# Performance work log

Measured on AMD Instinct MI355X. Metric: run time of the kernel, lower is better.

The kernel has to match this reference:

```python
import jax, jax.numpy as jnp
import numpy as np

OMEGA_ENC = 0.01   # Encoder.omega
OMEGA_K = 0.1      # KernelMLP.omega
N0, E0 = 4096, 16384     # level-0 graph
N1, E1 = 1024, 8192      # level-1 (pooled) graph
F_IN, H, LAT, DIM = 8, 64, 32, 3
F = H + DIM              # conv input features (x || pos)


def _glorot(key, shape):
    s = jnp.sqrt(2.0 / (shape[0] + shape[-1]))
    return (jax.random.normal(key, shape) * s).astype(jnp.float32)


def setup_inputs() -> dict:
    key = jax.random.key(0)
    ks = jax.random.split(key, 24)
    inp = {
        "x": jax.random.normal(ks[0], (N0, F_IN), jnp.float32),
        "pos": jax.random.normal(ks[1], (N0, DIM), jnp.float32),
        "edge_index": jax.random.randint(ks[2], (2, E0), 0, N0),
        "pool_edge_index1": jax.random.randint(ks[3], (2, E1), 0, N1),
        "pool_pos1": jax.random.normal(ks[4], (N1, DIM), jnp.float32),
        "pool_keep_idx0": jnp.sort(jax.random.randint(ks[5], (N1,), 0, N0)),
        "lin0_w": _glorot(ks[6], (F_IN, H)),
        "lin0_b": 0.01 * jax.random.normal(ks[7], (H,), jnp.float32),
        "lin1_w": _glorot(ks[8], (H, LAT)),
        "lin1_b": 0.01 * jax.random.normal(ks[9], (LAT,), jnp.float32),
    }
    k = 10
    for i in range(2):
        inp[f"conv{i}_k_w0"] = _glorot(ks[k], (DIM + 1, H))
        inp[f"conv{i}_k_b0"] = 0.01 * jax.random.normal(ks[k + 1], (H,), jnp.float32)
        inp[f"conv{i}_k_w1"] = _glorot(ks[k + 2], (H, H))
        inp[f"conv{i}_k_b1"] = 0.01 * jax.random.normal(ks[k + 3], (H,), jnp.float32)
        inp[f"conv{i}_k_w2"] = _glorot(ks[k + 4], (H, F))
        inp[f"conv{i}_k_b2"] = 0.01 * jax.random.normal(ks[k + 5], (F,), jnp.float32)
        inp[f"conv{i}_bias"] = jnp.zeros((H,), jnp.float32)  # zeros() init in torch
        k += 6
    return inp


def _with_self_loops(ei, n):
    # add_remaining_self_loops: input edges are assumed self-loop-free
    loops = jnp.arange(n, dtype=ei.dtype)
    return jnp.concatenate([ei, jnp.stack([loops, loops])], axis=1)


def _kernel_conv(xf, ei, pos, n, w0, b0, w1, b1, w2, b2, bias):
    src, dst = ei[0], ei[1]
    rel = pos[dst] - pos[src]                               # [E,3]
    zero = jnp.all(rel == 0.0, axis=1)                      # self loops -> rho=0, nan phi in torch
    rel_s = jnp.where(zero[:, None], 1.0, rel)              # safe values (avoid nan grads)
    rho = jnp.sqrt(jnp.sum(rel_s * rel_s, axis=1))
    theta = jnp.arctan2(rel_s[:, 1], rel_s[:, 0])
    phi = jnp.arcsin(jnp.clip(rel_s[:, 2] / rho, -1.0, 1.0))
    # torch sets theta/phi to 0 where phi is nan (rho==0); rho itself is 0 there
    rho = jnp.where(zero, 0.0, rho)
    theta = jnp.where(zero, 0.0, theta)
    phi = jnp.where(zero, 0.0, phi)
    feats = jnp.stack([rho, theta / jnp.pi, phi / jnp.pi], axis=1)   # [E,3]
    # KernelMLP lin0 on (feats || channel_id), evaluated for all out channels at once
    base = feats @ w0[:DIM] + b0                            # [E,H]
    ch = jnp.arange(H, dtype=xf.dtype)                      # out_channels == H
    h0 = jnp.sin(OMEGA_K * (base[None] + ch[:, None, None] * w0[DIM][None, None]))  # [C,E,H]
    h1 = jnp.sin(OMEGA_K * (jnp.einsum('ceh,hk->cek', h0, w1) + b1))                # [C,E,H]
    x_j = xf[src]                                           # [E,F]
    # msg[e,c] = (lin2(h1[c,e]) * x_j[e]).sum(); lin2 folded into the contraction
    msg = jnp.einsum('ceh,hf,ef->ec', h1, w2, x_j) + (x_j @ b2)[:, None]            # [E,C]
    return jax.ops.segment_sum(msg, dst, num_segments=n) + bias


def reference(x, edge_index, pos, pool_edge_index1, pool_pos1, pool_keep_idx0,
              lin0_w, lin0_b, lin1_w, lin1_b,
              conv0_k_w0, conv0_k_b0, conv0_k_w1, conv0_k_b1, conv0_k_w2, conv0_k_b2, conv0_bias,
              conv1_k_w0, conv1_k_b0, conv1_k_w1, conv1_k_b1, conv1_k_w2, conv1_k_b2, conv1_bias):
    n0 = x.shape[0]
    h = jnp.sin(OMEGA_ENC * (x @ lin0_w + lin0_b))
    ei0 = _with_self_loops(edge_index, n0)
    h = jnp.sin(OMEGA_ENC * _kernel_conv(jnp.concatenate([h, pos], 1), ei0, pos, n0,
                                         conv0_k_w0, conv0_k_b0, conv0_k_w1, conv0_k_b1,
                                         conv0_k_w2, conv0_k_b2, conv0_bias))
    # max_pool_neighbor_x: per-node max over neighbors incl. self (self loops in ei0)
    h = jax.ops.segment_max(h[ei0[0]], ei0[1], num_segments=n0)[pool_keep_idx0]
    n1 = pool_pos1.shape[0]
    ei1 = _with_self_loops(pool_edge_index1, n1)
    h = jnp.sin(OMEGA_ENC * _kernel_conv(jnp.concatenate([h, pool_pos1], 1), ei1, pool_pos1, n1,
                                         conv1_k_w0, conv1_k_b0, conv1_k_w1, conv1_k_b1,
                                         conv1_k_w2, conv1_k_b2, conv1_bias))
    return jnp.sin(OMEGA_ENC * (h @ lin1_w + lin1_b))   # [N1, LAT]
```

## Files before the change

kernel.cpp:

```cpp
#include <hip/hip_runtime.h>
#include <hip/hip_fp16.h>

#define N0C 4096
#define E0C 16384
#define N1C 1024
#define E1C 8192
#define HC 64
#define FINC 8
#define LATC 32
#define FC 67
#define E0T (E0C + N0C)
#define E1T (E1C + N1C)

typedef float f32x4 __attribute__((ext_vector_type(4)));
typedef _Float16 f16x8 __attribute__((ext_vector_type(8)));

__global__ __launch_bounds__(256) void k_prep(
    const float* __restrict__ x, const float* __restrict__ l0w,
    const float* __restrict__ l0b, const float* __restrict__ posp,
    const float* __restrict__ c0w2, const float* __restrict__ c0b2,
    const float* __restrict__ c0w0, const float* __restrict__ c1w0,
    const float* __restrict__ c0w1, const float* __restrict__ c1w1,
    _Float16* __restrict__ bC0, _Float16* __restrict__ bS0,
    _Float16* __restrict__ bC1, _Float16* __restrict__ bS1,
    _Float16* __restrict__ w1f0, _Float16* __restrict__ w1f1,
    float* __restrict__ tN, float* __restrict__ dN,
    float* __restrict__ accz) {
  if (blockIdx.x < 256) {
    __shared__ float w2s[64][69];
    __shared__ float xr[4][64];
    const int tid = threadIdx.x;
    const int wave = __builtin_amdgcn_readfirstlane(tid >> 6), lane = tid & 63;
    for (int idx = tid; idx < HC * FC; idx += 256)
      w2s[idx / FC][idx % FC] = c0w2[idx];
    __syncthreads();
#pragma unroll
    for (int i = 0; i < 4; ++i) {
      const int n = (blockIdx.x * 4 + wave) + i * 1024;
      float a = l0b[lane];
#pragma unroll
      for (int f = 0; f < FINC; ++f) a = fmaf(x[n * FINC + f], l0w[f * HC + lane], a);
      xr[wave][lane] = sinf(0.01f * a);
      __builtin_amdgcn_wave_barrier();
      const float px = posp[n * 3], py = posp[n * 3 + 1], pz = posp[n * 3 + 2];
      float tl = 0.f, ds = 0.f;
#pragma unroll 8
      for (int f = 0; f < HC; ++f) {
        float xv = xr[wave][f];
        tl = fmaf(xv, w2s[lane][f], tl);
        ds = fmaf(xv, c0b2[f], ds);
      }
      tl = fmaf(px, w2s[lane][64], fmaf(py, w2s[lane][65], fmaf(pz, w2s[lane][66], tl)));
      ds = fmaf(px, c0b2[64], fmaf(py, c0b2[65], fmaf(pz, c0b2[66], ds)));
      tN[n * HC + lane] = tl;
      if (lane == 0) dN[n] = ds;
      __builtin_amdgcn_wave_barrier();
    }
  } else if (blockIdx.x < 320) {
    int id = (blockIdx.x - 256) * 256 + threadIdx.x;
    if (id < 8192) {
      int lvl = id >> 12, r = id & 4095;
      int fi = r >> 9, lane = (r >> 3) & 63, j = r & 7;
      int nt = fi & 3, ks = fi >> 2;
      int c = nt * 16 + (lane & 15);
      int h = ks * 32 + (lane >> 4) * 8 + j;
      const float* w = lvl ? c1w0 : c0w0;
      float s, cv;
      sincosf(0.1f * (float)c * w[3 * HC + h], &s, &cv);
      (lvl ? bC1 : bC0)[r] = (_Float16)cv;
      (lvl ? bS1 : bS0)[r] = (_Float16)s;
    } else {
      int r0 = id - 8192;
      int lvl = r0 >> 12, r = r0 & 4095;
      int fi = r >> 9, lane = (r >> 3) & 63, j = r & 7;
      int ms = fi & 3, ks = fi >> 2;
      int h = ks * 32 + (lane >> 4) * 8 + j;
      int kout = ms * 16 + (lane & 15);
      const float* w = lvl ? c1w1 : c0w1;
      (lvl ? w1f1 : w1f0)[r] = (_Float16)(0.1f * w[h * HC + kout]);
    }
  } else {
    int t = (blockIdx.x - 320) * 256 + threadIdx.x;
    f32x4 z = {0.f, 0.f, 0.f, 0.f};
    f32x4* zp = (f32x4*)accz;
    zp[t] = z;
    zp[t + 49152] = z;
    zp[t + 98304] = z;
  }
}

template <bool L1>
__global__ __launch_bounds__(256, 3) void k_conv(
    const int* __restrict__ ei, int E, int eTot,
    const float* __restrict__ posp,
    const float* __restrict__ tN, const float* __restrict__ dN,
    const unsigned* __restrict__ pooled, const int* __restrict__ keep,
    const float* __restrict__ w2, const float* __restrict__ b2,
    const float* __restrict__ kw0, const float* __restrict__ kb0,
    const _Float16* __restrict__ bC, const _Float16* __restrict__ bS,
    const _Float16* __restrict__ w1f, const float* __restrict__ b1,
    float* __restrict__ acc_out) {
  __shared__ __attribute__((aligned(16))) _Float16 bCs[4096], bSs[4096];
  __shared__ __attribute__((aligned(16))) _Float16 scS[4][2][64], scC[4][2][64];
  __shared__ float w2s[64][69];
  __shared__ float xrs[4][2][64];
  __shared__ float trow[4][64];
  const int tid = threadIdx.x;
  const int wave = __builtin_amdgcn_readfirstlane(tid >> 6), lane = tid & 63;
  const int q = lane >> 4;
  for (int idx = tid; idx < 512; idx += 256) {
    ((f16x8*)bCs)[idx] = ((const f16x8*)bC)[idx];
    ((f16x8*)bSs)[idx] = ((const f16x8*)bS)[idx];
  }
  if constexpr (L1) {
    for (int idx = tid; idx < HC * FC; idx += 256)
      w2s[idx / FC][idx % FC] = w2[idx];
  }
  f16x8 w1r[8];
#pragma unroll
  for (int f = 0; f < 8; ++f) w1r[f] = *(const f16x8*)(w1f + ((f << 6) + lane) * 8);
  f32x4 bbq[4];
#pragma unroll
  for (int ms = 0; ms < 4; ++ms) {
    f32x4 t = *(const f32x4*)(b1 + ms * 16 + q * 4);
    bbq[ms] = t * 0.1f;
  }
  const float kb0v = kb0[lane];
  const float kw0x = kw0[lane], kw0y = kw0[HC + lane], kw0z = kw0[2 * HC + lane];
  float b2v = 0.f, b2x = 0.f, b2y = 0.f, b2z = 0.f;
  if constexpr (L1) {
    b2v = b2[lane];
    b2x = b2[64]; b2y = b2[65]; b2z = b2[66];
  }
  __syncthreads();

  const int nW = gridDim.x * 4;
  int e = blockIdx.x * 4 + wave;
  if (e >= eTot) return;

  auto stg = [&](int ee, int bufIdx, int& sN, int& dTo, float& sv, float& cv,
                 float& dv, float& opx, float& opy, float& opz) {
    int s, d2;
    if (ee < E) { s = ei[ee]; d2 = ei[E + ee]; } else { s = ee - E; d2 = s; }
    sN = s;
    dTo = d2;
    const float px = posp[s * 3], py = posp[s * 3 + 1], pz = posp[s * 3 + 2];
    const float rx = posp[d2 * 3] - px;
    const float ry = posp[d2 * 3 + 1] - py;
    const float rz = posp[d2 * 3 + 2] - pz;
    opx = px; opy = py; opz = pz;
    float f0 = 0.f, f1 = 0.f, f2 = 0.f;
    if (!(rx == 0.f && ry == 0.f && rz == 0.f)) {
      const float INV_PI = 0.3183098861837907f;
      const float PI_F = 3.14159265358979f;
      const float PI_2 = 1.5707963267948966f;
      float rho = sqrtf(rx * rx + ry * ry + rz * rz);
      float ax = fabsf(rx), ay = fabsf(ry);
      float mx = fmaxf(ax, ay), mn = fminf(ax, ay);
      float zr = mn * __builtin_amdgcn_rcpf(mx);
      float z2 = zr * zr;
      float pa = fmaf(z2, -0.0040540580f, 0.0218612288f);
      pa = fmaf(z2, pa, -0.0559098861f);
      pa = fmaf(z2, pa, 0.0964200441f);
      pa = fmaf(z2, pa, -0.1390853351f);
      pa = fmaf(z2, pa, 0.1994653599f);
      pa = fmaf(z2, pa, -0.3332985605f);
      pa = fmaf(z2, pa, 0.9999993329f);
      float at = pa * zr;
      at = (ay > ax) ? (PI_2 - at) : at;
      at = (rx < 0.f) ? (PI_F - at) : at;
      float th = copysignf(at, ry);
      float zz = rz * __builtin_amdgcn_rcpf(rho);
      float az = fminf(fabsf(zz), 1.0f);
      float sq = sqrtf(1.0f - az);
      float pp = fmaf(az, -0.0187293f, 0.0742610f);
      pp = fmaf(az, pp, -0.2121144f);
      pp = fmaf(az, pp, 1.5707288f);
      float as = PI_2 - sq * pp;
      float ph = copysignf(as, zz);
      f0 = rho; f1 = th * INV_PI; f2 = ph * INV_PI;
    }
    float base = fmaf(f0, kw0x, fmaf(f1, kw0y, fmaf(f2, kw0z, kb0v)));
    __sincosf(0.1f * base, &sv, &cv);
    if constexpr (L1) {
      int kn = keep[s];
      unsigned key = pooled[(size_t)kn * HC + lane];
      unsigned bb = (key & 0x80000000u) ? (key & 0x7FFFFFFFu) : ~key;
      float xv = __uint_as_float(bb);
      xrs[wave][bufIdx][lane] = xv;
      float dp = xv * b2v;
      dp += __shfl_xor(dp, 1, 64);  dp += __shfl_xor(dp, 2, 64);
      dp += __shfl_xor(dp, 4, 64);  dp += __shfl_xor(dp, 8, 64);
      dp += __shfl_xor(dp, 16, 64); dp += __shfl_xor(dp, 32, 64);
      dv = dp + fmaf(px, b2x, fmaf(py, b2y, pz * b2z));
    } else {
      dv = dN[s];
    }
  };

  int s0, d0;
  float sv0, cv0, dv0, p0x, p0y, p0z;
  stg(e, 0, s0, d0, sv0, cv0, dv0, p0x, p0y, p0z);
  int buf = 0;
  scS[wave][0][lane] = (_Float16)sv0;
  scC[wave][0][lane] = (_Float16)cv0;
  __builtin_amdgcn_wave_barrier();

  while (true) {
    const int en = e + nW;
    const bool more = en < eTot;
    int s1 = 0, d1 = 0;
    float sv1 = 0.f, cv1 = 0.f, dv1 = 0.f, p1x = 0.f, p1y = 0.f, p1z = 0.f;
    if (more) {
      stg(en, buf ^ 1, s1, d1, sv1, cv1, dv1, p1x, p1y, p1z);
      scS[wave][buf ^ 1][lane] = (_Float16)sv1;
      scC[wave][buf ^ 1][lane] = (_Float16)cv1;
    }
    __builtin_amdgcn_wave_barrier();

    f32x4 tr[4];
    if constexpr (L1) {
      float tl = 0.f;
#pragma unroll 8
      for (int f = 0; f < HC; ++f) tl = fmaf(xrs[wave][buf][f], w2s[lane][f], tl);
      tl = fmaf(p0x, w2s[lane][64],
           fmaf(p0y, w2s[lane][65], fmaf(p0z, w2s[lane][66], tl)));
      trow[wave][lane] = tl;
      __builtin_amdgcn_wave_barrier();
#pragma unroll
      for (int ms = 0; ms < 4; ++ms)
        tr[ms] = *(const f32x4*)&trow[wave][ms * 16 + q * 4];
      __builtin_amdgcn_wave_barrier();
    } else {
      const float* trp = tN + (size_t)s0 * HC;
#pragma unroll
      for (int ms = 0; ms < 4; ++ms) tr[ms] = *(const f32x4*)(trp + ms * 16 + q * 4);
    }

    f32x4 acc[4][4];
#pragma unroll
    for (int ms = 0; ms < 4; ++ms)
#pragma unroll
      for (int nt = 0; nt < 4; ++nt) acc[ms][nt] = bbq[ms];
#pragma unroll
    for (int ks = 0; ks < 2; ++ks) {
      f16x8 sv8 = *(const f16x8*)&scS[wave][buf][ks * 32 + q * 8];
      f16x8 cv8 = *(const f16x8*)&scC[wave][buf][ks * 32 + q * 8];
      f16x8 bf[4];
#pragma unroll
      for (int nt = 0; nt < 4; ++nt) {
        f16x8 cb = *(const f16x8*)&bCs[((ks * 4 + nt) * 64 + lane) * 8];
        f16x8 sb = *(const f16x8*)&bSs[((ks * 4 + nt) * 64 + lane) * 8];
        bf[nt] = sv8 * cb + cv8 * sb;
      }
#pragma unroll
      for (int ms = 0; ms < 4; ++ms)
#pragma unroll
        for (int nt = 0; nt < 4; ++nt)
          acc[ms][nt] = __builtin_amdgcn_mfma_f32_16x16x32_f16(
              w1r[ks * 4 + ms], bf[nt], acc[ms][nt], 0, 0, 0);
    }

    float snt0 = 0.f, snt1 = 0.f, snt2 = 0.f, snt3 = 0.f;
#pragma unroll
    for (int ms = 0; ms < 4; ++ms) {
#pragma unroll
      for (int r = 0; r < 4; ++r) {
        float tt = tr[ms][r];
        snt0 = fmaf(__sinf(acc[ms][0][r]), tt, snt0);
        snt1 = fmaf(__sinf(acc[ms][1][r]), tt, snt1);
        snt2 = fmaf(__sinf(acc[ms][2][r]), tt, snt2);
        snt3 = fmaf(__sinf(acc[ms][3][r]), tt, snt3);
      }
    }
    snt0 += __shfl_xor(snt0, 16, 64); snt0 += __shfl_xor(snt0, 32, 64);
    snt1 += __shfl_xor(snt1, 16, 64); snt1 += __shfl_xor(snt1, 32, 64);
    snt2 += __shfl_xor(snt2, 16, 64); snt2 += __shfl_xor(snt2, 32, 64);
    snt3 += __shfl_xor(snt3, 16, 64); snt3 += __shfl_xor(snt3, 32, 64);
    float val = (q == 0) ? snt0 : (q == 1) ? snt1 : (q == 2) ? snt2 : snt3;
    atomicAdd(acc_out + (size_t)d0 * HC + lane, val + dv0);

    if (!more) break;
    e = en; s0 = s1; d0 = d1; dv0 = dv1;
    p0x = p1x; p0y = p1y; p0z = p1z;
    buf ^= 1;
  }
}

__global__ __launch_bounds__(256) void k_pool(
    const int* __restrict__ ei, const float* __restrict__ acc0,
    const float* __restrict__ bias, unsigned int* __restrict__ pooled) {
  const int wave = threadIdx.x >> 6, lane = threadIdx.x & 63;
  const float bz = bias[lane];
  for (int e = blockIdx.x * 4 + wave; e < E0T; e += gridDim.x * 4) {
    int s, d;
    if (e < E0C) { s = ei[e]; d = ei[E0C + e]; } else { s = e - E0C; d = s; }
    float v = sinf(0.01f * (acc0[(size_t)s * HC + lane] + bz));
    unsigned int b = __float_as_uint(v);
    unsigned int key = (b & 0x80000000u) ? ~b : (b | 0x80000000u);
    atomicMax(pooled + (size_t)d * HC + lane, key);
  }
}

__global__ __launch_bounds__(256) void k_final(
    const float* __restrict__ acc1, const float* __restrict__ bias,
    const float* __restrict__ l1w, const float* __restrict__ l1b,
    float* __restrict__ outp) {
  __shared__ float hr[4][64];
  const int wave = threadIdx.x >> 6, lane = threadIdx.x & 63;
  const int node = blockIdx.x * 4 + wave;
  hr[wave][lane] = sinf(0.01f * (acc1[(size_t)node * HC + lane] + bias[lane]));
  __syncthreads();
  if (lane < LATC) {
    const float* h = hr[wave];
    float o = l1b[lane];
#pragma unroll 8
    for (int c = 0; c < HC; ++c) o = fmaf(h[c], l1w[c * LATC + lane], o);
    outp[node * LATC + lane] = sinf(0.01f * o);
  }
}

extern "C" void kernel_launch(void* const* d_in, const int* in_sizes, int n_in,
                              void* d_out, int out_size, void* d_ws, size_t ws_size,
                              hipStream_t stream) {
  (void)in_sizes; (void)n_in; (void)out_size; (void)ws_size;
  const float* x    = (const float*)d_in[0];
  const float* pos  = (const float*)d_in[1];
  const int*   ei   = (const int*)d_in[2];
  const int*   pei  = (const int*)d_in[3];
  const float* ppos = (const float*)d_in[4];
  const int*   keep = (const int*)d_in[5];
  const float* l0w  = (const float*)d_in[6];
  const float* l0b  = (const float*)d_in[7];
  const float* l1w  = (const float*)d_in[8];
  const float* l1b  = (const float*)d_in[9];
  const float* c0w0 = (const float*)d_in[10];
  const float* c0b0 = (const float*)d_in[11];
  const float* c0w1 = (const float*)d_in[12];
  const float* c0b1 = (const float*)d_in[13];
  const float* c0w2 = (const float*)d_in[14];
  const float* c0b2 = (const float*)d_in[15];
  const float* c0bias = (const float*)d_in[16];
  const float* c1w0 = (const float*)d_in[17];
  const float* c1b0 = (const float*)d_in[18];
  const float* c1w1 = (const float*)d_in[19];
  const float* c1b1 = (const float*)d_in[20];
  const float* c1w2 = (const float*)d_in[21];
  const float* c1b2 = (const float*)d_in[22];
  const float* c1bias = (const float*)d_in[23];
  float* outp = (float*)d_out;

  char* p = (char*)d_ws;
  auto carve = [&](size_t bytes) -> char* {
    char* r = p;
    p += (bytes + 255) & ~(size_t)255;
    return r;
  };
  float* tN0  = (float*)carve((size_t)N0C * HC * 4);
  float* dN0  = (float*)carve((size_t)N0C * 4);
  _Float16* bC0  = (_Float16*)carve(4096 * 2);
  _Float16* bS0  = (_Float16*)carve(4096 * 2);
  _Float16* bC1  = (_Float16*)carve(4096 * 2);
  _Float16* bS1  = (_Float16*)carve(4096 * 2);
  _Float16* w1f0 = (_Float16*)carve(4096 * 2);
  _Float16* w1f1 = (_Float16*)carve(4096 * 2);
  float* acc0 = (float*)carve((size_t)N0C * HC * 4);
  unsigned int* pooled = (unsigned int*)carve((size_t)N0C * HC * 4);
  float* acc1 = (float*)carve((size_t)N1C * HC * 4);

  k_prep<<<512, 256, 0, stream>>>(x, l0w, l0b, pos, c0w2, c0b2,
                                  c0w0, c1w0, c0w1, c1w1,
                                  bC0, bS0, bC1, bS1, w1f0, w1f1,
                                  tN0, dN0, acc0);
  k_conv<false><<<768, 256, 0, stream>>>(ei, E0C, E0T, pos, tN0, dN0,
                                         nullptr, nullptr, nullptr, nullptr,
                                         c0w0, c0b0, bC0, bS0, w1f0, c0b1, acc0);
  k_pool<<<1280, 256, 0, stream>>>(ei, acc0, c0bias, pooled);
  k_conv<true><<<768, 256, 0, stream>>>(pei, E1C, E1T, ppos, nullptr, nullptr,
                                        pooled, keep, c1w2, c1b2,
                                        c1w0, c1b0, bC1, bS1, w1f1, c1b1, acc1);
  k_final<<<N1C / 4, 256, 0, stream>>>(acc1, c1bias, l1w, l1b, outp);
}
```

Before: 163.7 us.

## Skip level-0 conv and pool work not reachable from kept nodes

An extra block in the prep kernel builds two byte maps from the keep indices, using a binary search over them for each edge. One marks kept nodes. The other marks nodes whose level-0 conv output feeds the max-pool into a kept node. The level-0 conv then skips, per wave, edges whose destination is not needed, and the pool kernel skips edges into non-kept nodes. This removes MFMA, sin and atomic work whose results are dropped by the gather at pool_keep_idx0. The cost is a small serial bitmap-building pass added to the prep launch.

After: 236.4 us. 1.44x slower.

```diff
diff --git a/kernel.cpp b/kernel.cpp
--- a/kernel.cpp
+++ b/kernel.cpp
@@ -21,11 +21,12 @@
     const float* __restrict__ c0w2, const float* __restrict__ c0b2,
     const float* __restrict__ c0w0, const float* __restrict__ c1w0,
     const float* __restrict__ c0w1, const float* __restrict__ c1w1,
+    const int* __restrict__ ei, const int* __restrict__ keep,
     _Float16* __restrict__ bC0, _Float16* __restrict__ bS0,
     _Float16* __restrict__ bC1, _Float16* __restrict__ bS1,
     _Float16* __restrict__ w1f0, _Float16* __restrict__ w1f1,
     float* __restrict__ tN, float* __restrict__ dN,
-    float* __restrict__ accz) {
+    float* __restrict__ accz, unsigned char* __restrict__ bitmaps) {
   if (blockIdx.x < 256) {
     __shared__ float w2s[64][69];
     __shared__ float xr[4][64];
@@ -79,13 +80,31 @@
       const float* w = lvl ? c1w1 : c0w1;
       (lvl ? w1f1 : w1f0)[r] = (_Float16)(0.1f * w[h * HC + kout]);
     }
-  } else {
+  } else if (blockIdx.x < 512) {
     int t = (blockIdx.x - 320) * 256 + threadIdx.x;
     f32x4 z = {0.f, 0.f, 0.f, 0.f};
     f32x4* zp = (f32x4*)accz;
     zp[t] = z;
     zp[t + 49152] = z;
     zp[t + 98304] = z;
+  } else {
+    __shared__ int ks[1024];
+    const int tid = threadIdx.x;
+    for (int i = tid; i < 1024; i += 256) ks[i] = keep[i];
+    for (int i = tid; i < 2048; i += 256) ((unsigned int*)bitmaps)[i] = 0u;
+    __syncthreads();
+    unsigned char* needed = bitmaps;
+    unsigned char* iskept = bitmaps + 4096;
+    for (int e = tid; e < E0T; e += 256) {
+      int s, d;
+      if (e < E0C) { s = ei[e]; d = ei[E0C + e]; } else { s = e - E0C; d = s; }
+      int lo = 0, hi = 1024;
+      while (hi - lo > 1) {
+        int mid = (lo + hi) >> 1;
+        if (ks[mid] <= d) lo = mid; else hi = mid;
+      }
+      if (ks[lo] == d) { needed[s] = 1; iskept[d] = 1; }
+    }
   }
 }
 
@@ -96,6 +115,7 @@
     const float* __restrict__ tN, const float* __restrict__ dN,
     const unsigned* __restrict__ pooled, const int* __restrict__ keep,
     const float* __restrict__ w2, const float* __restrict__ b2,
+    const unsigned char* __restrict__ ndmap,
     const float* __restrict__ kw0, const float* __restrict__ kb0,
     const _Float16* __restrict__ bC, const _Float16* __restrict__ bS,
     const _Float16* __restrict__ w1f, const float* __restrict__ b1,
@@ -138,12 +158,16 @@
   int e = blockIdx.x * 4 + wave;
   if (e >= eTot) return;
 
-  auto stg = [&](int ee, int bufIdx, int& sN, int& dTo, float& sv, float& cv,
-                 float& dv, float& opx, float& opy, float& opz) {
+  auto stg = [&](int ee, int bufIdx, int& sN, int& dTo, bool& act, float& sv,
+                 float& cv, float& dv, float& opx, float& opy, float& opz) {
     int s, d2;
     if (ee < E) { s = ei[ee]; d2 = ei[E + ee]; } else { s = ee - E; d2 = s; }
     sN = s;
     dTo = d2;
+    act = true;
+    if constexpr (!L1) act = (ndmap[d2] != 0);
+    sv = 0.f; cv = 0.f; dv = 0.f; opx = 0.f; opy = 0.f; opz = 0.f;
+    if (!act) return;
     const float px = posp[s * 3], py = posp[s * 3 + 1], pz = posp[s * 3 + 2];
     const float rx = posp[d2 * 3] - px;
     const float ry = posp[d2 * 3 + 1] - py;
@@ -199,8 +223,9 @@
   };
 
   int s0, d0;
+  bool act0;
   float sv0, cv0, dv0, p0x, p0y, p0z;
-  stg(e, 0, s0, d0, sv0, cv0, dv0, p0x, p0y, p0z);
+  stg(e, 0, s0, d0, act0, sv0, cv0, dv0, p0x, p0y, p0z);
   int buf = 0;
   scS[wave][0][lane] = (_Float16)sv0;
   scC[wave][0][lane] = (_Float16)cv0;
@@ -210,78 +235,81 @@
     const int en = e + nW;
     const bool more = en < eTot;
     int s1 = 0, d1 = 0;
+    bool act1 = false;
     float sv1 = 0.f, cv1 = 0.f, dv1 = 0.f, p1x = 0.f, p1y = 0.f, p1z = 0.f;
     if (more) {
-      stg(en, buf ^ 1, s1, d1, sv1, cv1, dv1, p1x, p1y, p1z);
+      stg(en, buf ^ 1, s1, d1, act1, sv1, cv1, dv1, p1x, p1y, p1z);
       scS[wave][buf ^ 1][lane] = (_Float16)sv1;
       scC[wave][buf ^ 1][lane] = (_Float16)cv1;
     }
     __builtin_amdgcn_wave_barrier();
 
-    f32x4 tr[4];
-    if constexpr (L1) {
-      float tl = 0.f;
+    if (act0) {
+      f32x4 tr[4];
+      if constexpr (L1) {
+        float tl = 0.f;
 #pragma unroll 8
-      for (int f = 0; f < HC; ++f) tl = fmaf(xrs[wave][buf][f], w2s[lane][f], tl);
-      tl = fmaf(p0x, w2s[lane][64],
-           fmaf(p0y, w2s[lane][65], fmaf(p0z, w2s[lane][66], tl)));
-      trow[wave][lane] = tl;
-      __builtin_amdgcn_wave_barrier();
+        for (int f = 0; f < HC; ++f) tl = fmaf(xrs[wave][buf][f], w2s[lane][f], tl);
+        tl = fmaf(p0x, w2s[lane][64],
+             fmaf(p0y, w2s[lane][65], fmaf(p0z, w2s[lane][66], tl)));
+        trow[wave][lane] = tl;
+        __builtin_amdgcn_wave_barrier();
+#pragma unroll
+        for (int ms = 0; ms < 4; ++ms)
+          tr[ms] = *(const f32x4*)&trow[wave][ms * 16 + q * 4];
+        __builtin_amdgcn_wave_barrier();
+      } else {
+        const float* trp = tN + (size_t)s0 * HC;
+#pragma unroll
+        for (int ms = 0; ms < 4; ++ms) tr[ms] = *(const f32x4*)(trp + ms * 16 + q * 4);
+      }
+
+      f32x4 acc[4][4];
 #pragma unroll
       for (int ms = 0; ms < 4; ++ms)
-        tr[ms] = *(const f32x4*)&trow[wave][ms * 16 + q * 4];
-      __builtin_amdgcn_wave_barrier();
-    } else {
-      const float* trp = tN + (size_t)s0 * HC;
-#pragma unroll
-      for (int ms = 0; ms < 4; ++ms) tr[ms] = *(const f32x4*)(trp + ms * 16 + q * 4);
-    }
-
-    f32x4 acc[4][4];
-#pragma unroll
-    for (int ms = 0; ms < 4; ++ms)
-#pragma unroll
-      for (int nt = 0; nt < 4; ++nt) acc[ms][nt] = bbq[ms];
-#pragma unroll
-    for (int ks = 0; ks < 2; ++ks) {
-      f16x8 sv8 = *(const f16x8*)&scS[wave][buf][ks * 32 + q * 8];
-      f16x8 cv8 = *(const f16x8*)&scC[wave][buf][ks * 32 + q * 8];
-      f16x8 bf[4];
-#pragma unroll
-      for (int nt = 0; nt < 4; ++nt) {
-        f16x8 cb = *(const f16x8*)&bCs[((ks * 4 + nt) * 64 + lane) * 8];
-        f16x8 sb = *(const f16x8*)&bSs[((ks * 4 + nt) * 64 + lane) * 8];
-        bf[nt] = sv8 * cb + cv8 * sb;
+#pragma unroll
+        for (int nt = 0; nt < 4; ++nt) acc[ms][nt] = bbq[ms];
+#pragma unroll
+      for (int ks = 0; ks < 2; ++ks) {
+        f16x8 sv8 = *(const f16x8*)&scS[wave][buf][ks * 32 + q * 8];
+        f16x8 cv8 = *(const f16x8*)&scC[wave][buf][ks * 32 + q * 8];
+        f16x8 bf[4];
+#pragma unroll
+        for (int nt = 0; nt < 4; ++nt) {
+          f16x8 cb = *(const f16x8*)&bCs[((ks * 4 + nt) * 64 + lane) * 8];
+          f16x8 sb = *(const f16x8*)&bSs[((ks * 4 + nt) * 64 + lane) * 8];
+          bf[nt] = sv8 * cb + cv8 * sb;
+        }
+#pragma unroll
+        for (int ms = 0; ms < 4; ++ms)
+#pragma unroll
+          for (int nt = 0; nt < 4; ++nt)
+            acc[ms][nt] = __builtin_amdgcn_mfma_f32_16x16x32_f16(
+                w1r[ks * 4 + ms], bf[nt], acc[ms][nt], 0, 0, 0);
       }
-#pragma unroll
-      for (int ms = 0; ms < 4; ++ms)
-#pragma unroll
-        for (int nt = 0; nt < 4; ++nt)
-          acc[ms][nt] = __builtin_amdgcn_mfma_f32_16x16x32_f16(
-              w1r[ks * 4 + ms], bf[nt], acc[ms][nt], 0, 0, 0);
-    }
-
-    float snt0 = 0.f, snt1 = 0.f, snt2 = 0.f, snt3 = 0.f;
-#pragma unroll
-    for (int ms = 0; ms < 4; ++ms) {
-#pragma unroll
-      for (int r = 0; r < 4; ++r) {
-        float tt = tr[ms][r];
-        snt0 = fmaf(__sinf(acc[ms][0][r]), tt, snt0);
-        snt1 = fmaf(__sinf(acc[ms][1][r]), tt, snt1);
-        snt2 = fmaf(__sinf(acc[ms][2][r]), tt, snt2);
-        snt3 = fmaf(__sinf(acc[ms][3][r]), tt, snt3);
+
+      float snt0 = 0.f, snt1 = 0.f, snt2 = 0.f, snt3 = 0.f;
+#pragma unroll
+      for (int ms = 0; ms < 4; ++ms) {
+#pragma unroll
+        for (int r = 0; r < 4; ++r) {
+          float tt = tr[ms][r];
+          snt0 = fmaf(__sinf(acc[ms][0][r]), tt, snt0);
+          snt1 = fmaf(__sinf(acc[ms][1][r]), tt, snt1);
+          snt2 = fmaf(__sinf(acc[ms][2][r]), tt, snt2);
+          snt3 = fmaf(__sinf(acc[ms][3][r]), tt, snt3);
+        }
       }
-    }
-    snt0 += __shfl_xor(snt0, 16, 64); snt0 += __shfl_xor(snt0, 32, 64);
-    snt1 += __shfl_xor(snt1, 16, 64); snt1 += __shfl_xor(snt1, 32, 64);
-    snt2 += __shfl_xor(snt2, 16, 64); snt2 += __shfl_xor(snt2, 32, 64);
-    snt3 += __shfl_xor(snt3, 16, 64); snt3 += __shfl_xor(snt3, 32, 64);
-    float val = (q == 0) ? snt0 : (q == 1) ? snt1 : (q == 2) ? snt2 : snt3;
-    atomicAdd(acc_out + (size_t)d0 * HC + lane, val + dv0);
+      snt0 += __shfl_xor(snt0, 16, 64); snt0 += __shfl_xor(snt0, 32, 64);
+      snt1 += __shfl_xor(snt1, 16, 64); snt1 += __shfl_xor(snt1, 32, 64);
+      snt2 += __shfl_xor(snt2, 16, 64); snt2 += __shfl_xor(snt2, 32, 64);
+      snt3 += __shfl_xor(snt3, 16, 64); snt3 += __shfl_xor(snt3, 32, 64);
+      float val = (q == 0) ? snt0 : (q == 1) ? snt1 : (q == 2) ? snt2 : snt3;
+      atomicAdd(acc_out + (size_t)d0 * HC + lane, val + dv0);
+    }
 
     if (!more) break;
-    e = en; s0 = s1; d0 = d1; dv0 = dv1;
+    e = en; s0 = s1; d0 = d1; act0 = act1; dv0 = dv1;
     p0x = p1x; p0y = p1y; p0z = p1z;
     buf ^= 1;
   }
@@ -289,12 +317,14 @@
 
 __global__ __launch_bounds__(256) void k_pool(
     const int* __restrict__ ei, const float* __restrict__ acc0,
-    const float* __restrict__ bias, unsigned int* __restrict__ pooled) {
+    const float* __restrict__ bias, const unsigned char* __restrict__ iskept,
+    unsigned int* __restrict__ pooled) {
   const int wave = threadIdx.x >> 6, lane = threadIdx.x & 63;
   const float bz = bias[lane];
   for (int e = blockIdx.x * 4 + wave; e < E0T; e += gridDim.x * 4) {
     int s, d;
     if (e < E0C) { s = ei[e]; d = ei[E0C + e]; } else { s = e - E0C; d = s; }
+    if (!iskept[d]) continue;
     float v = sinf(0.01f * (acc0[(size_t)s * HC + lane] + bz));
     unsigned int b = __float_as_uint(v);
     unsigned int key = (b & 0x80000000u) ? ~b : (b | 0x80000000u);
@@ -367,17 +397,19 @@
   float* acc0 = (float*)carve((size_t)N0C * HC * 4);
   unsigned int* pooled = (unsigned int*)carve((size_t)N0C * HC * 4);
   float* acc1 = (float*)carve((size_t)N1C * HC * 4);
-
-  k_prep<<<512, 256, 0, stream>>>(x, l0w, l0b, pos, c0w2, c0b2,
-                                  c0w0, c1w0, c0w1, c1w1,
+  unsigned char* bitmaps = (unsigned char*)carve(8192);
+
+  k_prep<<<513, 256, 0, stream>>>(x, l0w, l0b, pos, c0w2, c0b2,
+                                  c0w0, c1w0, c0w1, c1w1, ei, keep,
                                   bC0, bS0, bC1, bS1, w1f0, w1f1,
-                                  tN0, dN0, acc0);
+                                  tN0, dN0, acc0, bitmaps);
   k_conv<false><<<768, 256, 0, stream>>>(ei, E0C, E0T, pos, tN0, dN0,
                                          nullptr, nullptr, nullptr, nullptr,
+                                         bitmaps,
                                          c0w0, c0b0, bC0, bS0, w1f0, c0b1, acc0);
-  k_pool<<<1280, 256, 0, stream>>>(ei, acc0, c0bias, pooled);
+  k_pool<<<1280, 256, 0, stream>>>(ei, acc0, c0bias, bitmaps + 4096, pooled);
   k_conv<true><<<768, 256, 0, stream>>>(pei, E1C, E1T, ppos, nullptr, nullptr,
-                                        pooled, keep, c1w2, c1b2,
+                                        pooled, keep, c1w2, c1b2, nullptr,
                                         c1w0, c1b0, bC1, bS1, w1f1, c1b1, acc1);
   k_final<<<N1C / 4, 256, 0, stream>>>(acc1, c1bias, l1w, l1b, outp);
 }
```
